# Kernel tuning notes

Hardware: AMD Instinct MI355X
Metric: run time of the kernel (lower is better)

The kernel has to match this reference:

```python
import jax, jax.numpy as jnp
import numpy as np

H = 8  # num_heads

def layer_norm(x, g, b, eps=1e-5):
    mu = x.mean(-1, keepdims=True)
    var = ((x - mu) ** 2).mean(-1, keepdims=True)
    return (x - mu) / jnp.sqrt(var + eps) * g + b

def setup_inputs() -> dict:
    key = jax.random.key(0)
    ks = jax.random.split(key, 8)
    T, B, E, F = 64, 32, 512, 2048
    std = 0.02
    return {
        "x": jax.random.normal(ks[0], (T, B, E), jnp.float32),
        "relation": jax.random.normal(ks[1], (T, T, B, E), jnp.float32),
        "in_w": jax.random.normal(ks[2], (3 * E, E), jnp.float32) * std,
        "in_b": jnp.zeros((3 * E,), jnp.float32),
        "rel_w": jax.random.normal(ks[3], (E, 2 * E), jnp.float32) * std,
        "rel_b": jnp.zeros((2 * E,), jnp.float32),
        "out_w": jax.random.normal(ks[4], (E, E), jnp.float32) * std,
        "out_b": jnp.zeros((E,), jnp.float32),
        "fc1_w": jax.random.normal(ks[5], (E, F), jnp.float32) * std,
        "fc1_b": jnp.zeros((F,), jnp.float32),
        "fc2_w": jax.random.normal(ks[6], (F, E), jnp.float32) * std,
        "fc2_b": jnp.zeros((E,), jnp.float32),
        "ln1_g": jnp.ones((E,), jnp.float32),
        "ln1_b": jnp.zeros((E,), jnp.float32),
        "ln2_g": jnp.ones((E,), jnp.float32),
        "ln2_b": jnp.zeros((E,), jnp.float32),
    }

def reference(x, relation, in_w, in_b, rel_w, rel_b, out_w, out_b,
              fc1_w, fc1_b, fc2_w, fc2_b, ln1_g, ln1_b, ln2_g, ln2_b):
    T, B, E = x.shape
    Dh = E // H
    scaling = Dh ** -0.5
    # qkv projection (F.linear with weight [3E, E])
    qkv = x @ in_w.T + in_b                      # (T, B, 3E)
    q, k, v = jnp.split(qkv, 3, axis=-1)
    q = q.reshape(T, B * H, Dh)
    k = k.reshape(T, B * H, Dh)
    v = v.reshape(T, B * H, Dh)
    # relation bias: Conv1D(2E, E) -> ra, rb, view+transpose(0,1) as in torch
    r = relation @ rel_w + rel_b                 # (T, T, B, 2E)
    ra, rb = jnp.split(r, 2, axis=-1)
    ra = jnp.swapaxes(ra.reshape(T, T, B * H, Dh), 0, 1)
    rb = jnp.swapaxes(rb.reshape(T, T, B * H, Dh), 0, 1)
    # (q + ra) scaled, elementwise-reduce against (k + rb), extra 1/sqrt(Dh)
    q2 = (q[:, None] + ra) * scaling             # (T, T, BH, Dh)
    k2 = k[None, :] + rb                         # (T, T, BH, Dh)
    w = jnp.einsum('ijbn,ijbn->ijb', q2, k2) * scaling  # (T, T, BH)
    w = jax.nn.softmax(w, axis=1)                # softmax over src dim
    attn = jnp.einsum('ijb,jbn->bin', w, v)      # (BH, T, Dh)
    attn = jnp.swapaxes(attn, 0, 1).reshape(T, B, E)
    attn = attn @ out_w + out_b
    h = layer_norm(x + attn, ln1_g, ln1_b)
    f = jax.nn.relu(h @ fc1_w + fc1_b) @ fc2_w + fc2_b
    return layer_norm(h + f, ln2_g, ln2_b)
```

## Files before the change

### kernel.cpp

```cpp
#include <hip/hip_runtime.h>


typedef __bf16 bf16;
typedef __attribute__((ext_vector_type(8))) __bf16 bf16x8;
typedef __attribute__((ext_vector_type(4))) __bf16 bf16x4;
typedef __attribute__((ext_vector_type(4))) float f32x4;

__device__ __forceinline__ void gl_lds16(const bf16* g, bf16* l) {
  __builtin_amdgcn_global_load_lds((const __attribute__((address_space(1))) void*)g,
                                   (__attribute__((address_space(3))) void*)l, 16, 0, 0);
}

__device__ __forceinline__ void block_sync_lds() {
  asm volatile("s_waitcnt lgkmcnt(0)" ::: "memory");
  __builtin_amdgcn_s_barrier();
  asm volatile("" ::: "memory");
}


template <int NSRC, int NT>
__device__ __forceinline__ void convkn(int t, const float* __restrict__ W,
                                       bf16* __restrict__ dst) {
  int frag = t >> 5, r = t & 31;
  int lh = r >> 3, j = r & 7;
  int kt = frag / NT, nt = frag - kt * NT;
  int k = kt * 32 + lh * 8 + j;
  const float* src = W + (long)k * NSRC + nt * 16;
  f32x4 v0 = ((const f32x4*)src)[0], v1 = ((const f32x4*)src)[1];
  f32x4 v2 = ((const f32x4*)src)[2], v3 = ((const f32x4*)src)[3];
  bf16* d = dst + frag * 512 + lh * 128 + j;
  d[0] = (bf16)v0[0];  d[8] = (bf16)v0[1];  d[16] = (bf16)v0[2];  d[24] = (bf16)v0[3];
  d[32] = (bf16)v1[0]; d[40] = (bf16)v1[1]; d[48] = (bf16)v1[2];  d[56] = (bf16)v1[3];
  d[64] = (bf16)v2[0]; d[72] = (bf16)v2[1]; d[80] = (bf16)v2[2];  d[88] = (bf16)v2[3];
  d[96] = (bf16)v3[0]; d[104] = (bf16)v3[1]; d[112] = (bf16)v3[2]; d[120] = (bf16)v3[3];
}

__global__ void prep_kernel(const float* __restrict__ x,
                            const float* __restrict__ in_w,
                            const float* __restrict__ rel_w,
                            const float* __restrict__ out_w,
                            const float* __restrict__ fc1_w,
                            const float* __restrict__ fc2_w,
                            bf16* __restrict__ x_b,
                            bf16* __restrict__ inw_fl,
                            bf16* __restrict__ relw_fl,
                            bf16* __restrict__ outw_fl,
                            bf16* __restrict__ fc1w_fl,
                            bf16* __restrict__ fc2w_fl) {
  int t = blockIdx.x * 256 + threadIdx.x;
  if (t < 131072) {
    int d0 = t * 8;
    f32x4 a = *(const f32x4*)(x + d0), b = *(const f32x4*)(x + d0 + 4);
    bf16x8 r;
    r[0] = (bf16)a[0]; r[1] = (bf16)a[1]; r[2] = (bf16)a[2]; r[3] = (bf16)a[3];
    r[4] = (bf16)b[0]; r[5] = (bf16)b[1]; r[6] = (bf16)b[2]; r[7] = (bf16)b[3];
    *(bf16x8*)(x_b + d0) = r;
    return;
  }
  t -= 131072;
  if (t < 98304) {
    int d0 = t * 8;
    int frag = d0 >> 9, l = t & 63;
    int kt = frag / 96, nt = frag - kt * 96;
    const float* src = in_w + (long)(nt * 16 + (l & 15)) * 512 + kt * 32 + ((l >> 4) << 3);
    f32x4 a = *(const f32x4*)src, b = *(const f32x4*)(src + 4);
    bf16x8 r;
    r[0] = (bf16)a[0]; r[1] = (bf16)a[1]; r[2] = (bf16)a[2]; r[3] = (bf16)a[3];
    r[4] = (bf16)b[0]; r[5] = (bf16)b[1]; r[6] = (bf16)b[2]; r[7] = (bf16)b[3];
    *(bf16x8*)(inw_fl + d0) = r;
    return;
  }
  t -= 98304;
  if (t < 32768) { convkn<1024, 64>(t, rel_w, relw_fl); return; }
  t -= 32768;
  if (t < 16384) { convkn<512, 32>(t, out_w, outw_fl); return; }
  t -= 16384;
  if (t < 65536) { convkn<2048, 128>(t, fc1_w, fc1w_fl); return; }
  t -= 65536;
  if (t < 65536) { convkn<512, 32>(t, fc2_w, fc2w_fl); }
}

template <int WM, int WN, int MT, int NT, bool RELU, bool WF32, bool WBF16>
__global__ __launch_bounds__(256, 2) void gemm_bf16(
    const bf16* __restrict__ A, const bf16* __restrict__ Bfl,
    const float* __restrict__ bias, float* __restrict__ Cf,
    bf16* __restrict__ Cb, int M, int N, int K) {
  constexpr int AFR = WM * MT;
  constexpr int BFR = WN * NT;
  constexpr int NA = AFR / 4, NB = BFR / 4;
  __shared__ __align__(16) bf16 lA[2][AFR * 512];
  __shared__ __align__(16) bf16 lB[2][BFR * 512];
  const int tid = threadIdx.x, l = tid & 63, wv = tid >> 6;
  const int wm = wv / WN, wn = wv % WN;
  const int m0 = blockIdx.x * (AFR * 16), n0 = blockIdx.y * (BFR * 16);
  const int NTfr = N >> 4, nb0 = n0 >> 4, KT = K >> 5;

  f32x4 acc[MT][NT];
#pragma unroll
  for (int i = 0; i < MT; i++)
#pragma unroll
    for (int j = 0; j < NT; j++) acc[i][j] = (f32x4)0.f;

  const bf16* pA[NA];
#pragma unroll
  for (int i = 0; i < NA; ++i) {
    int f = wv + i * 4;
    pA[i] = A + (long)(m0 + f * 16 + (l & 15)) * K + ((l >> 4) << 3);
  }
  const bf16* pB[NB];
#pragma unroll
  for (int i = 0; i < NB; ++i) {
    int f = wv + i * 4;
    pB[i] = Bfl + (long)(nb0 + f) * 512 + l * 8;
  }
#pragma unroll
  for (int i = 0; i < NA; ++i) gl_lds16(pA[i], &lA[0][(wv + i * 4) * 512]);
#pragma unroll
  for (int i = 0; i < NB; ++i) gl_lds16(pB[i], &lB[0][(wv + i * 4) * 512]);

  for (int kt = 0; kt < KT; ++kt) {
    const int buf = kt & 1;
    __syncthreads();
    if (kt + 1 < KT) {
#pragma unroll
      for (int i = 0; i < NA; ++i)
        gl_lds16(pA[i] + (kt + 1) * 32, &lA[buf ^ 1][(wv + i * 4) * 512]);
#pragma unroll
      for (int i = 0; i < NB; ++i)
        gl_lds16(pB[i] + (long)(kt + 1) * NTfr * 512, &lB[buf ^ 1][(wv + i * 4) * 512]);
    }
    bf16x8 af[MT], bfr[NT];
#pragma unroll
    for (int mt = 0; mt < MT; ++mt)
      af[mt] = *(const bf16x8*)(&lA[buf][(wm * MT + mt) * 512 + l * 8]);
#pragma unroll
    for (int nt = 0; nt < NT; ++nt)
      bfr[nt] = *(const bf16x8*)(&lB[buf][(wn * NT + nt) * 512 + l * 8]);
#pragma unroll
    for (int mt = 0; mt < MT; ++mt)
#pragma unroll
      for (int nt = 0; nt < NT; ++nt)
        acc[mt][nt] = __builtin_amdgcn_mfma_f32_16x16x32_bf16(af[mt], bfr[nt],
                                                              acc[mt][nt], 0, 0, 0);
  }
#pragma unroll
  for (int nt = 0; nt < NT; nt++) {
    int n = n0 + (wn * NT + nt) * 16 + (l & 15);
    float bv = bias[n];
#pragma unroll
    for (int mt = 0; mt < MT; mt++) {
#pragma unroll
      for (int j = 0; j < 4; j++) {
        int row = m0 + (wm * MT + mt) * 16 + ((l >> 4) << 2) + j;
        float v = acc[mt][nt][j] + bv;
        if (RELU) v = fmaxf(v, 0.f);
        if (WF32) Cf[(long)row * N + n] = v;
        if (WBF16) Cb[(long)row * N + n] = (bf16)v;
      }
    }
  }
}

#define RELW_STEP(kt_, buf_, BC, BN, STG_W, STG_P)                               \
  {                                                                              \
    bf16x4 cv;                                                                   \
    cv[0] = (bf16)STG_W[0]; cv[1] = (bf16)STG_W[1];                              \
    cv[2] = (bf16)STG_W[2]; cv[3] = (bf16)STG_W[3];                              \
    *(bf16x4*)(&lA[buf_][adst]) = cv;                                            \
    block_sync_lds();                                                            \
    if ((kt_) + 2 < 16) STG_P = *(const f32x4*)(asrc + ((kt_) + 2) * 32);        \
    if ((kt_) + 1 < 16) {                                                        \
      _Pragma("unroll") for (int f = 0; f < 8; ++f)                              \
          BN[f] = *(const bf16x8*)(relw_fl + (long)((kt_) + 1) * 32768 + boff0 + \
                                   (((f >> 2) * 32 + (f & 3)) << 9));            \
    }                                                                            \
    bf16x8 af[4];                                                                \
    _Pragma("unroll") for (int mt = 0; mt < 4; mt++)                             \
        af[mt] = *(const bf16x8*)(&lA[buf_][mt * 512 + l * 8]);                  \
    _Pragma("unroll") for (int mt = 0; mt < 4; mt++)                             \
        _Pragma("unroll") for (int ns = 0; ns < 8; ns++)                         \
            acc[mt][ns] = __builtin_amdgcn_mfma_f32_16x16x32_bf16(               \
                af[mt], BC[ns], acc[mt][ns], 0, 0, 0);                           \
  }

__global__ __launch_bounds__(512, 2) void relw_kernel(
    const float* __restrict__ rel, const bf16* __restrict__ relw_fl,
    const float* __restrict__ rel_b, const float* __restrict__ qkv,
    float* __restrict__ wT) {
  __shared__ __align__(16) bf16 lA[2][2048];
  const int tid = threadIdx.x;
  const int l = tid & 63;
  const int h = tid >> 6;
  const int t1 = blockIdx.x >> 5;
  const int r2 = blockIdx.x & 31;
  const long row0 = ((long)t1 * 64 + r2 * 2) * 32;

  f32x4 acc[4][8];
#pragma unroll
  for (int i = 0; i < 4; i++)
#pragma unroll
    for (int j = 0; j < 8; j++) acc[i][j] = (f32x4)0.f;

  const int slot = tid >> 1, half = tid & 1;
  const int fA = slot >> 6, l2 = slot & 63;
  const float* asrc =
      rel + (row0 + fA * 16 + (l2 & 15)) * 512 + ((l2 >> 4) << 3) + half * 4;
  const int adst = fA * 512 + l2 * 8 + half * 4;

  const int boff0 = h * 2048 + l * 8;

  f32x4 stgA = *(const f32x4*)asrc;
  f32x4 stgB = *(const f32x4*)(asrc + 32);
  bf16x8 b0[8], b1[8];
#pragma unroll
  for (int f = 0; f < 8; ++f)
    b0[f] = *(const bf16x8*)(relw_fl + boff0 + (((f >> 2) * 32 + (f & 3)) << 9));

  for (int kt = 0; kt < 16; kt += 2) {
    RELW_STEP(kt, 0, b0, b1, stgA, stgA)
    RELW_STEP(kt + 1, 1, b1, b0, stgB, stgB)
  }

  const int dhb = h * 64;
#pragma unroll
  for (int mt = 0; mt < 4; mt++) {
    float psum[4] = {0.f, 0.f, 0.f, 0.f};
#pragma unroll
    for (int nt = 0; nt < 4; nt++) {
      const int dh = nt * 16 + (l & 15);
      const float ba = rel_b[dhb + dh];
      const float bb2 = rel_b[512 + dhb + dh];
#pragma unroll
      for (int j = 0; j < 4; j++) {
        int rl = mt * 16 + ((l >> 4) << 2) + j;
        int b = rl & 31;
        int t2 = r2 * 2 + (rl >> 5);
        float qv = qkv[(long)(t2 * 32 + b) * 1536 + dhb + dh];
        float kv = qkv[(long)(t1 * 32 + b) * 1536 + 512 + dhb + dh];
        psum[j] += (qv + acc[mt][nt][j] + ba) * (kv + acc[mt][nt + 4][j] + bb2);
      }
    }
#pragma unroll
    for (int j = 0; j < 4; j++) {
      float v = psum[j];
      v += __shfl_xor(v, 1);
      v += __shfl_xor(v, 2);
      v += __shfl_xor(v, 4);
      v += __shfl_xor(v, 8);
      if ((l & 15) == 0) {
        int rl = mt * 16 + ((l >> 4) << 2) + j;
        int b = rl & 31;
        int i = r2 * 2 + (rl >> 5);
        wT[(long)(i * 256 + b * 8 + h) * 64 + t1] = v * 0.015625f;
      }
    }
  }
}

__global__ __launch_bounds__(256) void attn_kernel(const float* __restrict__ wT,
                                                   const float* __restrict__ qkv,
                                                   bf16* __restrict__ attn_b) {
  __shared__ __align__(16) float s[64][68];
  __shared__ __align__(16) float vl[64][68];
  __shared__ float pm[64][4], ps[64][4];
  const int tid = threadIdx.x;
  const int b = blockIdx.x >> 3, h = blockIdx.x & 7;
  const int i = tid >> 2, g = tid & 3;

  const float* wsrc = wT + ((long)i * 256 + b * 8 + h) * 64 + g * 16;
  f32x4 w0 = ((const f32x4*)wsrc)[0], w1 = ((const f32x4*)wsrc)[1];
  f32x4 w2 = ((const f32x4*)wsrc)[2], w3 = ((const f32x4*)wsrc)[3];
  const float* vsrc = qkv + ((long)i * 32 + b) * 1536 + 1024 + h * 64 + g * 16;
  f32x4 v0 = ((const f32x4*)vsrc)[0], v1 = ((const f32x4*)vsrc)[1];
  f32x4 v2 = ((const f32x4*)vsrc)[2], v3 = ((const f32x4*)vsrc)[3];
  *(f32x4*)&vl[i][g * 16] = v0;
  *(f32x4*)&vl[i][g * 16 + 4] = v1;
  *(f32x4*)&vl[i][g * 16 + 8] = v2;
  *(f32x4*)&vl[i][g * 16 + 12] = v3;
  float pmax = -1e30f;
#pragma unroll
  for (int u = 0; u < 4; ++u) {
    pmax = fmaxf(pmax, fmaxf(fmaxf(w0[u], w1[u]), fmaxf(w2[u], w3[u])));
  }
  pm[i][g] = pmax;
  __syncthreads();
  float m = fmaxf(fmaxf(pm[i][0], pm[i][1]), fmaxf(pm[i][2], pm[i][3]));
  float psum = 0.f;
  f32x4 e0, e1, e2, e3;
#pragma unroll
  for (int u = 0; u < 4; ++u) {
    e0[u] = __expf(w0[u] - m); psum += e0[u];
    e1[u] = __expf(w1[u] - m); psum += e1[u];
    e2[u] = __expf(w2[u] - m); psum += e2[u];
    e3[u] = __expf(w3[u] - m); psum += e3[u];
  }
  *(f32x4*)&s[i][g * 16] = e0;
  *(f32x4*)&s[i][g * 16 + 4] = e1;
  *(f32x4*)&s[i][g * 16 + 8] = e2;
  *(f32x4*)&s[i][g * 16 + 12] = e3;
  ps[i][g] = psum;
  __syncthreads();
  float scale = 1.f / (ps[i][0] + ps[i][1] + ps[i][2] + ps[i][3]);
  f32x4 o0 = (f32x4)0.f, o1 = (f32x4)0.f, o2 = (f32x4)0.f, o3 = (f32x4)0.f;
  for (int j = 0; j < 64; ++j) {
    float pj = s[i][j];
    const float* vr = &vl[j][g * 16];
    f32x4 a0 = ((const f32x4*)vr)[0], a1 = ((const f32x4*)vr)[1];
    f32x4 a2 = ((const f32x4*)vr)[2], a3 = ((const f32x4*)vr)[3];
#pragma unroll
    for (int u = 0; u < 4; ++u) {
      o0[u] = fmaf(pj, a0[u], o0[u]);
      o1[u] = fmaf(pj, a1[u], o1[u]);
      o2[u] = fmaf(pj, a2[u], o2[u]);
      o3[u] = fmaf(pj, a3[u], o3[u]);
    }
  }
  bf16x8 r0, r1;
#pragma unroll
  for (int u = 0; u < 4; ++u) {
    r0[u] = (bf16)(o0[u] * scale);
    r0[4 + u] = (bf16)(o1[u] * scale);
    r1[u] = (bf16)(o2[u] * scale);
    r1[4 + u] = (bf16)(o3[u] * scale);
  }
  bf16* dst = attn_b + ((long)i * 32 + b) * 512 + h * 64 + g * 16;
  *(bf16x8*)dst = r0;
  *(bf16x8*)(dst + 8) = r1;
}

template <bool WB>
__global__ __launch_bounds__(256) void ln_kernel(const float* __restrict__ a,
                                                 const float* __restrict__ res,
                                                 const float* __restrict__ g,
                                                 const float* __restrict__ bb,
                                                 float* __restrict__ of,
                                                 bf16* __restrict__ ob) {
  const int l = threadIdx.x & 63;
  const int row = blockIdx.x * 4 + (threadIdx.x >> 6);
  const float* pa = a + (long)row * 512;
  const float* pr = res + (long)row * 512;
  float xv[8];
  float s = 0.f, sq = 0.f;
#pragma unroll
  for (int u = 0; u < 8; ++u) {
    xv[u] = pa[u * 64 + l] + pr[u * 64 + l];
    s += xv[u];
    sq += xv[u] * xv[u];
  }
#pragma unroll
  for (int st = 1; st < 64; st <<= 1) {
    s += __shfl_xor(s, st);
    sq += __shfl_xor(sq, st);
  }
  float mean = s * (1.f / 512.f);
  float var = sq * (1.f / 512.f) - mean * mean;
  float rstd = rsqrtf(var + 1e-5f);
#pragma unroll
  for (int u = 0; u < 8; ++u) {
    int e = u * 64 + l;
    float v = (xv[u] - mean) * rstd * g[e] + bb[e];
    of[(long)row * 512 + e] = v;
    if (WB) ob[(long)row * 512 + e] = (bf16)v;
  }
}

extern "C" void kernel_launch(void* const* d_in, const int* in_sizes, int n_in,
                              void* d_out, int out_size, void* d_ws, size_t ws_size,
                              hipStream_t stream) {
  const float* x     = (const float*)d_in[0];
  const float* rel   = (const float*)d_in[1];
  const float* in_w  = (const float*)d_in[2];
  const float* in_b  = (const float*)d_in[3];
  const float* rel_w = (const float*)d_in[4];
  const float* rel_b = (const float*)d_in[5];
  const float* out_w = (const float*)d_in[6];
  const float* out_b = (const float*)d_in[7];
  const float* fc1_w = (const float*)d_in[8];
  const float* fc1_b = (const float*)d_in[9];
  const float* fc2_w = (const float*)d_in[10];
  const float* fc2_b = (const float*)d_in[11];
  const float* ln1_g = (const float*)d_in[12];
  const float* ln1_b = (const float*)d_in[13];
  const float* ln2_g = (const float*)d_in[14];
  const float* ln2_b = (const float*)d_in[15];

  char* ws = (char*)d_ws;
  float* qkv   = (float*)(ws + 0);
  bf16* x_b    = (bf16*)(ws + 12582912);
  bf16* inw    = (bf16*)(ws + 14680064);
  bf16* relwB  = (bf16*)(ws + 16252928);
  bf16* outwB  = (bf16*)(ws + 17301504);
  bf16* fc1wB  = (bf16*)(ws + 17825792);
  bf16* fc2wB  = (bf16*)(ws + 19922944);
  float* wT    = (float*)(ws + 22020096);
  bf16* attn   = (bf16*)(ws + 26214400);
  float* opre  = (float*)(ws + 28311552);
  float* hf    = (float*)(ws + 32505856);
  bf16* hb     = (bf16*)(ws + 36700160);
  bf16* fb     = (bf16*)(ws + 38797312);
  float* f2o   = (float*)(ws + 47185920);

  prep_kernel<<<1600, 256, 0, stream>>>(x, in_w, rel_w, out_w, fc1_w, fc2_w,
                                        x_b, inw, relwB, outwB, fc1wB, fc2wB);
  gemm_bf16<2, 2, 2, 4, false, true, false><<<dim3(32, 12), 256, 0, stream>>>(
      x_b, inw, in_b, qkv, nullptr, 2048, 1536, 512);
  relw_kernel<<<2048, 512, 0, stream>>>(rel, relwB, rel_b, qkv, wT);
  attn_kernel<<<256, 256, 0, stream>>>(wT, qkv, attn);
  gemm_bf16<2, 2, 2, 2, false, true, false><<<dim3(32, 8), 256, 0, stream>>>(
      attn, outwB, out_b, opre, nullptr, 2048, 512, 512);
  ln_kernel<true><<<512, 256, 0, stream>>>(opre, x, ln1_g, ln1_b, hf, hb);
  gemm_bf16<2, 2, 4, 4, true, false, true><<<dim3(16, 16), 256, 0, stream>>>(
      hb, fc1wB, fc1_b, nullptr, fb, 2048, 2048, 512);
  gemm_bf16<2, 2, 2, 2, false, true, false><<<dim3(32, 8), 256, 0, stream>>>(
      fb, fc2wB, fc2_b, f2o, nullptr, 2048, 512, 2048);
  ln_kernel<false><<<512, 256, 0, stream>>>(f2o, hf, ln2_g, ln2_b, (float*)d_out,
                                            nullptr);
}
```

Before: 648.9 us.

## Retile relation GEMM with LDS-staged weights and cross-wave epilogue exchange

Restructures the dominant relation-projection kernel. Each 1024-thread block now takes a 128-row tile and half the output columns (4 heads), and the rel_w tiles are loaded into double-buffered LDS with global_load_lds instead of per-wave register loads. Each wave now holds only 16 accumulators. The ra/rb pairing for the q·k reduction is done through a shared-memory exchange between partner waves. The aim is to cut redundant weight traffic and register pressure and to raise occupancy, but each rel tile row is now converted twice (once per column half) and a larger shared-memory footprint is added.

```diff
diff --git a/kernel.cpp b/kernel.cpp
--- a/kernel.cpp
+++ b/kernel.cpp
@@ -9,12 +9,6 @@
 __device__ __forceinline__ void gl_lds16(const bf16* g, bf16* l) {
   __builtin_amdgcn_global_load_lds((const __attribute__((address_space(1))) void*)g,
                                    (__attribute__((address_space(3))) void*)l, 16, 0, 0);
-}
-
-__device__ __forceinline__ void block_sync_lds() {
-  asm volatile("s_waitcnt lgkmcnt(0)" ::: "memory");
-  __builtin_amdgcn_s_barrier();
-  asm volatile("" ::: "memory");
 }
 
 
@@ -161,97 +155,122 @@
   }
 }
 
-#define RELW_STEP(kt_, buf_, BC, BN, STG_W, STG_P)                               \
-  {                                                                              \
-    bf16x4 cv;                                                                   \
-    cv[0] = (bf16)STG_W[0]; cv[1] = (bf16)STG_W[1];                              \
-    cv[2] = (bf16)STG_W[2]; cv[3] = (bf16)STG_W[3];                              \
-    *(bf16x4*)(&lA[buf_][adst]) = cv;                                            \
-    block_sync_lds();                                                            \
-    if ((kt_) + 2 < 16) STG_P = *(const f32x4*)(asrc + ((kt_) + 2) * 32);        \
-    if ((kt_) + 1 < 16) {                                                        \
-      _Pragma("unroll") for (int f = 0; f < 8; ++f)                              \
-          BN[f] = *(const bf16x8*)(relw_fl + (long)((kt_) + 1) * 32768 + boff0 + \
-                                   (((f >> 2) * 32 + (f & 3)) << 9));            \
-    }                                                                            \
-    bf16x8 af[4];                                                                \
-    _Pragma("unroll") for (int mt = 0; mt < 4; mt++)                             \
-        af[mt] = *(const bf16x8*)(&lA[buf_][mt * 512 + l * 8]);                  \
-    _Pragma("unroll") for (int mt = 0; mt < 4; mt++)                             \
-        _Pragma("unroll") for (int ns = 0; ns < 8; ns++)                         \
-            acc[mt][ns] = __builtin_amdgcn_mfma_f32_16x16x32_bf16(               \
-                af[mt], BC[ns], acc[mt][ns], 0, 0, 0);                           \
-  }
-
-__global__ __launch_bounds__(512, 2) void relw_kernel(
+__global__ __launch_bounds__(1024, 4) void relw_kernel(
     const float* __restrict__ rel, const bf16* __restrict__ relw_fl,
-    const float* __restrict__ rel_b, const float* __restrict__ qkv,
+    const float* __restrict__ rel_bias, const float* __restrict__ qkv,
     float* __restrict__ wT) {
-  __shared__ __align__(16) bf16 lA[2][2048];
-  const int tid = threadIdx.x;
-  const int l = tid & 63;
-  const int h = tid >> 6;
-  const int t1 = blockIdx.x >> 5;
-  const int r2 = blockIdx.x & 31;
-  const long row0 = ((long)t1 * 64 + r2 * 2) * 32;
-
-  f32x4 acc[4][8];
+  __shared__ __align__(16) union U {
+    struct { bf16 A[2][8 * 512]; bf16 B[2][32 * 512]; } s;
+    float post[16][2048];
+  } u;
+  const int tid = threadIdx.x, l = tid & 63, w = tid >> 6;
+  const int mh = w >> 3, nq = w & 7;
+  const int tile = blockIdx.x >> 1, c = blockIdx.x & 1;
+  const int t1 = tile >> 4;
+  const int fb0 = (nq < 4) ? nq * 4 : 16 + (nq - 4) * 4;
+
+  f32x4 acc[4][4];
 #pragma unroll
   for (int i = 0; i < 4; i++)
 #pragma unroll
-    for (int j = 0; j < 8; j++) acc[i][j] = (f32x4)0.f;
-
-  const int slot = tid >> 1, half = tid & 1;
-  const int fA = slot >> 6, l2 = slot & 63;
-  const float* asrc =
-      rel + (row0 + fA * 16 + (l2 & 15)) * 512 + ((l2 >> 4) << 3) + half * 4;
-  const int adst = fA * 512 + l2 * 8 + half * 4;
-
-  const int boff0 = h * 2048 + l * 8;
-
-  f32x4 stgA = *(const f32x4*)asrc;
-  f32x4 stgB = *(const f32x4*)(asrc + 32);
-  bf16x8 b0[8], b1[8];
-#pragma unroll
-  for (int f = 0; f < 8; ++f)
-    b0[f] = *(const bf16x8*)(relw_fl + boff0 + (((f >> 2) * 32 + (f & 3)) << 9));
-
-  for (int kt = 0; kt < 16; kt += 2) {
-    RELW_STEP(kt, 0, b0, b1, stgA, stgA)
-    RELW_STEP(kt + 1, 1, b1, b0, stgB, stgB)
-  }
-
-  const int dhb = h * 64;
-#pragma unroll
-  for (int mt = 0; mt < 4; mt++) {
+    for (int j = 0; j < 4; j++) acc[i][j] = (f32x4)0.f;
+
+  const int sfm = tid >> 7;
+  const int slane = (tid >> 1) & 63;
+  const int sj = (tid & 1) * 4;
+  const int srow = tile * 128 + sfm * 16 + (slane & 15);
+  const int skof = ((slane >> 4) << 3) + sj;
+  const float* asrc = rel + (long)srow * 512 + skof;
+  const int adst = sfm * 512 + slane * 8 + sj;
+
+  const bf16* bsrc1 = relw_fl + ((long)(c * 16 + w)) * 512 + l * 8;
+  const bf16* bsrc2 = relw_fl + ((long)(32 + c * 16 + w)) * 512 + l * 8;
+
+  {
+    f32x4 a0 = *(const f32x4*)asrc;
+    bf16x4 cv;
+    cv[0] = (bf16)a0[0]; cv[1] = (bf16)a0[1]; cv[2] = (bf16)a0[2]; cv[3] = (bf16)a0[3];
+    *(bf16x4*)(&u.s.A[0][adst]) = cv;
+    gl_lds16(bsrc1, &u.s.B[0][w * 512]);
+    gl_lds16(bsrc2, &u.s.B[0][(16 + w) * 512]);
+  }
+  f32x4 stg = *(const f32x4*)(asrc + 32);
+
+  for (int kt = 0; kt < 16; ++kt) {
+    const int buf = kt & 1;
+    __syncthreads();
+    if (kt + 1 < 16) {
+      gl_lds16(bsrc1 + (long)(kt + 1) * 32768, &u.s.B[buf ^ 1][w * 512]);
+      gl_lds16(bsrc2 + (long)(kt + 1) * 32768, &u.s.B[buf ^ 1][(16 + w) * 512]);
+      bf16x4 cv;
+      cv[0] = (bf16)stg[0]; cv[1] = (bf16)stg[1]; cv[2] = (bf16)stg[2]; cv[3] = (bf16)stg[3];
+      *(bf16x4*)(&u.s.A[buf ^ 1][adst]) = cv;
+      if (kt + 2 < 16) stg = *(const f32x4*)(asrc + (kt + 2) * 32);
+    }
+    bf16x8 af[4];
+#pragma unroll
+    for (int mt = 0; mt < 4; ++mt)
+      af[mt] = *(const bf16x8*)(&u.s.A[buf][(mh * 4 + mt) * 512 + l * 8]);
+#pragma unroll
+    for (int nt = 0; nt < 4; ++nt) {
+      bf16x8 bf = *(const bf16x8*)(&u.s.B[buf][(fb0 + nt) * 512 + l * 8]);
+#pragma unroll
+      for (int mt = 0; mt < 4; ++mt)
+        acc[mt][nt] = __builtin_amdgcn_mfma_f32_16x16x32_bf16(af[mt], bf,
+                                                              acc[mt][nt], 0, 0, 0);
+    }
+  }
+
+  __syncthreads();
+  {
+    float* dst = &u.post[w][0];
+#pragma unroll
+    for (int mt2 = 0; mt2 < 2; ++mt2) {
+      int mt = (nq < 4) ? (2 + mt2) : mt2;
+#pragma unroll
+      for (int nt = 0; nt < 4; ++nt)
+        *(f32x4*)&dst[(mt2 * 4 + nt) * 256 + l * 4] = acc[mt][nt];
+    }
+  }
+  __syncthreads();
+
+  const int hq = nq & 3, h = c * 4 + hq, dhb = h * 64;
+  const int wp = (nq < 4) ? (w + 4) : (w - 4);
+  const int mtbase = (nq < 4) ? 0 : 2;
+  const int tt = tile & 15;
+#pragma unroll
+  for (int mt2 = 0; mt2 < 2; ++mt2) {
+    int mt = mtbase + mt2;
     float psum[4] = {0.f, 0.f, 0.f, 0.f};
 #pragma unroll
-    for (int nt = 0; nt < 4; nt++) {
-      const int dh = nt * 16 + (l & 15);
-      const float ba = rel_b[dhb + dh];
-      const float bb2 = rel_b[512 + dhb + dh];
-#pragma unroll
-      for (int j = 0; j < 4; j++) {
-        int rl = mt * 16 + ((l >> 4) << 2) + j;
-        int b = rl & 31;
-        int t2 = r2 * 2 + (rl >> 5);
-        float qv = qkv[(long)(t2 * 32 + b) * 1536 + dhb + dh];
-        float kv = qkv[(long)(t1 * 32 + b) * 1536 + 512 + dhb + dh];
-        psum[j] += (qv + acc[mt][nt][j] + ba) * (kv + acc[mt][nt + 4][j] + bb2);
+    for (int nt = 0; nt < 4; ++nt) {
+      int dh = nt * 16 + (l & 15);
+      float ba = rel_bias[dhb + dh];
+      float bb = rel_bias[512 + dhb + dh];
+      f32x4 part = *(const f32x4*)&u.post[wp][(mt2 * 4 + nt) * 256 + l * 4];
+      f32x4 rav, rbv;
+      if (nq < 4) { rav = acc[mt][nt]; rbv = part; }
+      else        { rav = part;        rbv = acc[mt][nt]; }
+#pragma unroll
+      for (int j = 0; j < 4; ++j) {
+        int rl = mh * 64 + mt * 16 + ((l >> 4) << 2) + j;
+        int t2b = tt * 128 + rl;
+        float qv = qkv[(long)t2b * 1536 + dhb + dh];
+        float kv = qkv[(long)(t1 * 32 + (rl & 31)) * 1536 + 512 + dhb + dh];
+        psum[j] += (qv + rav[j] + ba) * (kv + rbv[j] + bb);
       }
     }
 #pragma unroll
-    for (int j = 0; j < 4; j++) {
+    for (int j = 0; j < 4; ++j) {
       float v = psum[j];
       v += __shfl_xor(v, 1);
       v += __shfl_xor(v, 2);
       v += __shfl_xor(v, 4);
       v += __shfl_xor(v, 8);
       if ((l & 15) == 0) {
-        int rl = mt * 16 + ((l >> 4) << 2) + j;
-        int b = rl & 31;
-        int i = r2 * 2 + (rl >> 5);
-        wT[(long)(i * 256 + b * 8 + h) * 64 + t1] = v * 0.015625f;
+        int rl = mh * 64 + mt * 16 + ((l >> 4) << 2) + j;
+        int t2b = tt * 128 + rl;
+        wT[((long)t2b * 8 + h) * 64 + t1] = v * 0.015625f;
       }
     }
   }
@@ -279,8 +298,8 @@
   *(f32x4*)&vl[i][g * 16 + 12] = v3;
   float pmax = -1e30f;
 #pragma unroll
-  for (int u = 0; u < 4; ++u) {
-    pmax = fmaxf(pmax, fmaxf(fmaxf(w0[u], w1[u]), fmaxf(w2[u], w3[u])));
+  for (int uu = 0; uu < 4; ++uu) {
+    pmax = fmaxf(pmax, fmaxf(fmaxf(w0[uu], w1[uu]), fmaxf(w2[uu], w3[uu])));
   }
   pm[i][g] = pmax;
   __syncthreads();
@@ -288,11 +307,11 @@
   float psum = 0.f;
   f32x4 e0, e1, e2, e3;
 #pragma unroll
-  for (int u = 0; u < 4; ++u) {
-    e0[u] = __expf(w0[u] - m); psum += e0[u];
-    e1[u] = __expf(w1[u] - m); psum += e1[u];
-    e2[u] = __expf(w2[u] - m); psum += e2[u];
-    e3[u] = __expf(w3[u] - m); psum += e3[u];
+  for (int uu = 0; uu < 4; ++uu) {
+    e0[uu] = __expf(w0[uu] - m); psum += e0[uu];
+    e1[uu] = __expf(w1[uu] - m); psum += e1[uu];
+    e2[uu] = __expf(w2[uu] - m); psum += e2[uu];
+    e3[uu] = __expf(w3[uu] - m); psum += e3[uu];
   }
   *(f32x4*)&s[i][g * 16] = e0;
   *(f32x4*)&s[i][g * 16 + 4] = e1;
@@ -308,20 +327,20 @@
     f32x4 a0 = ((const f32x4*)vr)[0], a1 = ((const f32x4*)vr)[1];
     f32x4 a2 = ((const f32x4*)vr)[2], a3 = ((const f32x4*)vr)[3];
 #pragma unroll
-    for (int u = 0; u < 4; ++u) {
-      o0[u] = fmaf(pj, a0[u], o0[u]);
-      o1[u] = fmaf(pj, a1[u], o1[u]);
-      o2[u] = fmaf(pj, a2[u], o2[u]);
-      o3[u] = fmaf(pj, a3[u], o3[u]);
+    for (int uu = 0; uu < 4; ++uu) {
+      o0[uu] = fmaf(pj, a0[uu], o0[uu]);
+      o1[uu] = fmaf(pj, a1[uu], o1[uu]);
+      o2[uu] = fmaf(pj, a2[uu], o2[uu]);
+      o3[uu] = fmaf(pj, a3[uu], o3[uu]);
     }
   }
   bf16x8 r0, r1;
 #pragma unroll
-  for (int u = 0; u < 4; ++u) {
-    r0[u] = (bf16)(o0[u] * scale);
-    r0[4 + u] = (bf16)(o1[u] * scale);
-    r1[u] = (bf16)(o2[u] * scale);
-    r1[4 + u] = (bf16)(o3[u] * scale);
+  for (int uu = 0; uu < 4; ++uu) {
+    r0[uu] = (bf16)(o0[uu] * scale);
+    r0[4 + uu] = (bf16)(o1[uu] * scale);
+    r1[uu] = (bf16)(o2[uu] * scale);
+    r1[4 + uu] = (bf16)(o3[uu] * scale);
   }
   bf16* dst = attn_b + ((long)i * 32 + b) * 512 + h * 64 + g * 16;
   *(bf16x8*)dst = r0;
@@ -342,10 +361,10 @@
   float xv[8];
   float s = 0.f, sq = 0.f;
 #pragma unroll
-  for (int u = 0; u < 8; ++u) {
-    xv[u] = pa[u * 64 + l] + pr[u * 64 + l];
-    s += xv[u];
-    sq += xv[u] * xv[u];
+  for (int uu = 0; uu < 8; ++uu) {
+    xv[uu] = pa[uu * 64 + l] + pr[uu * 64 + l];
+    s += xv[uu];
+    sq += xv[uu] * xv[uu];
   }
 #pragma unroll
   for (int st = 1; st < 64; st <<= 1) {
@@ -356,9 +375,9 @@
   float var = sq * (1.f / 512.f) - mean * mean;
   float rstd = rsqrtf(var + 1e-5f);
 #pragma unroll
-  for (int u = 0; u < 8; ++u) {
-    int e = u * 64 + l;
-    float v = (xv[u] - mean) * rstd * g[e] + bb[e];
+  for (int uu = 0; uu < 8; ++uu) {
+    int e = uu * 64 + l;
+    float v = (xv[uu] - mean) * rstd * g[e] + bb[e];
     of[(long)row * 512 + e] = v;
     if (WB) ob[(long)row * 512 + e] = (bf16)v;
   }
@@ -404,7 +423,7 @@
                                         x_b, inw, relwB, outwB, fc1wB, fc2wB);
   gemm_bf16<2, 2, 2, 4, false, true, false><<<dim3(32, 12), 256, 0, stream>>>(
       x_b, inw, in_b, qkv, nullptr, 2048, 1536, 512);
-  relw_kernel<<<2048, 512, 0, stream>>>(rel, relwB, rel_b, qkv, wT);
+  relw_kernel<<<2048, 1024, 0, stream>>>(rel, relwB, rel_b, qkv, wT);
   attn_kernel<<<256, 256, 0, stream>>>(wT, qkv, attn);
   gemm_bf16<2, 2, 2, 2, false, true, false><<<dim3(32, 8), 256, 0, stream>>>(
       attn, outwB, out_b, opre, nullptr, 2048, 512, 512);
```

Result: slower. 2.163 ms (+233.3%).
